# Kernel optimization log

Hardware: AMD Instinct MI355X
Metric: run time of the kernel (lower is better)

Reference implementation:

```python
import jax, jax.numpy as jnp
import numpy as np

N_NODES = 50000
N_EDGES = 800000
N_GRAPHS = 64
D_IN = 96
D_HID = 96
D_OUT = 2
NEG_SLOPE = 0.2


def setup_inputs() -> dict:
    key = jax.random.key(0)
    ks = jax.random.split(key, 9)
    x = jax.random.normal(ks[0], (N_NODES, D_IN), dtype=jnp.float32)
    edge_index = jax.random.randint(ks[1], (2, N_EDGES), 0, N_NODES, dtype=jnp.int32)
    batch = jnp.sort(jax.random.randint(ks[2], (N_NODES,), 0, N_GRAPHS, dtype=jnp.int32))
    s1 = 1.0 / np.sqrt(D_IN)
    s2 = 1.0 / np.sqrt(D_HID)
    W1 = jax.random.normal(ks[3], (D_IN, D_HID), dtype=jnp.float32) * s1
    b1 = jnp.zeros((D_HID,), dtype=jnp.float32)
    W2 = jax.random.normal(ks[4], (D_HID, D_HID), dtype=jnp.float32) * s2
    b2 = jnp.zeros((D_HID,), dtype=jnp.float32)
    Wc = jax.random.normal(ks[5], (D_HID, D_OUT), dtype=jnp.float32) * s2
    bc = jnp.zeros((D_OUT,), dtype=jnp.float32)
    return {"x": x, "edge_index": edge_index, "batch": batch,
            "W1": W1, "b1": b1, "W2": W2, "b2": b2, "Wc": Wc, "bc": bc}


def _gcn_conv(h, W, b, src, dst, n_nodes):
    # GCNConv (Kipf): add self-loops, symmetric deg^-1/2 normalization.
    hW = h @ W  # [N, F]
    deg = jnp.zeros((n_nodes,), dtype=hW.dtype).at[dst].add(1.0) + 1.0  # +1 self-loop
    dinv = jax.lax.rsqrt(deg)
    coef = (dinv[src] * dinv[dst])[:, None]            # [E, 1]
    agg = jnp.zeros_like(hW).at[dst].add(hW[src] * coef)
    out = agg + hW * (dinv * dinv)[:, None] + b        # self-loop term: deg^-1 * hW
    return out


def _leaky(h):
    return jnp.where(h > 0, h, NEG_SLOPE * h)


def reference(x, edge_index, batch, W1, b1, W2, b2, Wc, bc):
    src, dst = edge_index[0], edge_index[1]
    h = _leaky(_gcn_conv(x, W1, b1, src, dst, N_NODES))
    h = _leaky(_gcn_conv(h, W2, b2, src, dst, N_NODES))
    # global_mean_pool over graph ids
    sums = jax.ops.segment_sum(h, batch, num_segments=N_GRAPHS)
    cnts = jax.ops.segment_sum(jnp.ones((N_NODES,), dtype=h.dtype), batch, num_segments=N_GRAPHS)
    pooled = sums / jnp.maximum(cnts, 1.0)[:, None]    # [G, F]
    return pooled @ Wc + bc                             # [G, D_OUT]
```

## Files before the change

### kernel.cpp

```cpp
#include <hip/hip_runtime.h>
#include <hip/hip_fp16.h>

#define NN 50000
#define NE 800000
#define NG 64
#define DF 96
#define SLOPE 0.2f
#define NBK 196
#define EB 196

using half8 = __attribute__((ext_vector_type(8))) _Float16;
using f32x4 = __attribute__((ext_vector_type(4))) float;

__global__ __launch_bounds__(256) void k_hist(const int* __restrict__ dst,
                                              int* __restrict__ hist2d) {
  __shared__ int h[NBK];
  int t = threadIdx.x;
  if (t < NBK) h[t] = 0;
  __syncthreads();
  int base = blockIdx.x * 4096;
  for (int k = 0; k < 16; ++k) {
    int e = base + k * 256 + t;
    if (e < NE) atomicAdd(&h[dst[e] >> 8], 1);
  }
  __syncthreads();
  if (t < NBK) hist2d[blockIdx.x * NBK + t] = h[t];
}

__global__ __launch_bounds__(256) void k_colscan(const int* __restrict__ hist2d,
                                                 int* __restrict__ colpref,
                                                 int* __restrict__ coltotal,
                                                 const int* __restrict__ batch,
                                                 int* __restrict__ gstart) {
  __shared__ int s[256];
  int col = blockIdx.x;
  int b = threadIdx.x;
  int v = (b < EB) ? hist2d[b * NBK + col] : 0;
  s[b] = v;
  __syncthreads();
  for (int o = 1; o < 256; o <<= 1) {
    int u = (b >= o) ? s[b - o] : 0;
    __syncthreads();
    s[b] += u;
    __syncthreads();
  }
  if (b < EB) colpref[b * NBK + col] = s[b] - v;
  if (b == 255) coltotal[col] = s[b];
  if (blockIdx.x == 0 && b <= NG) {
    int g = b, lo = 0, hi = NN;
    while (lo < hi) {
      int mid = (lo + hi) >> 1;
      if (batch[mid] < g) lo = mid + 1; else hi = mid;
    }
    gstart[g] = lo;
  }
}

__global__ __launch_bounds__(256) void k_bin2(const int* __restrict__ src,
                                              const int* __restrict__ dst,
                                              const int* __restrict__ hist2d,
                                              const int* __restrict__ coltotal,
                                              const int* __restrict__ colpref,
                                              int* __restrict__ binned) {
  __shared__ int h[NBK], loff[NBK], cur[NBK], gb[NBK];
  __shared__ int tmp[256];
  __shared__ int stage[4096];
  __shared__ unsigned char sbk[4096];
  int t = threadIdx.x;
  int ctv = (t < NBK) ? coltotal[t] : 0;
  tmp[t] = ctv;
  __syncthreads();
  for (int o = 1; o < 256; o <<= 1) {
    int u = (t >= o) ? tmp[t - o] : 0;
    __syncthreads();
    tmp[t] += u;
    __syncthreads();
  }
  int bbase_t = tmp[t] - ctv;
  if (t < NBK) h[t] = hist2d[blockIdx.x * NBK + t];
  __syncthreads();
  tmp[t] = (t < NBK) ? h[t] : 0;
  __syncthreads();
  for (int o = 1; o < 256; o <<= 1) {
    int u = (t >= o) ? tmp[t - o] : 0;
    __syncthreads();
    tmp[t] += u;
    __syncthreads();
  }
  if (t < NBK) {
    int excl = tmp[t] - h[t];
    loff[t] = excl;
    cur[t] = excl;
    gb[t] = bbase_t + colpref[blockIdx.x * NBK + t];
  }
  __syncthreads();
  int base = blockIdx.x * 4096;
  for (int k = 0; k < 16; ++k) {
    int e = base + k * 256 + t;
    if (e < NE) {
      int d = dst[e];
      int b = d >> 8;
      int p = atomicAdd(&cur[b], 1);
      stage[p] = src[e] | ((d & 255) << 16);
      sbk[p] = (unsigned char)b;
    }
  }
  __syncthreads();
  int tot = min(4096, NE - base);
  for (int i = t; i < tot; i += 256) {
    int b = sbk[i];
    binned[gb[b] + (i - loff[b])] = stage[i];
  }
}

__global__ __launch_bounds__(256) void k_csr(const int* __restrict__ binned,
                                             const int* __restrict__ coltotal,
                                             float* __restrict__ dinv,
                                             int* __restrict__ row_start,
                                             unsigned short* __restrict__ csr_src,
                                             float* __restrict__ partial) {
  __shared__ int h[256], cur[256], tmp[256];
  int t = threadIdx.x;
  int b = blockIdx.x;
  if (b == 0)
    for (int i = t; i < NG * DF; i += 256) partial[i] = 0.f;
  int ctv = (t < NBK) ? coltotal[t] : 0;
  h[t] = ctv;
  tmp[t] = ctv;
  __syncthreads();
  for (int o = 1; o < 256; o <<= 1) {
    int u = (t >= o) ? tmp[t - o] : 0;
    __syncthreads();
    tmp[t] += u;
    __syncthreads();
  }
  int ebeg = tmp[b] - h[b];
  int eend = tmp[b];
  __syncthreads();
  h[t] = 0;
  __syncthreads();
  for (int i = ebeg + t; i < eend; i += 256) atomicAdd(&h[(unsigned)binned[i] >> 16], 1);
  __syncthreads();
  tmp[t] = h[t];
  __syncthreads();
  for (int o = 1; o < 256; o <<= 1) {
    int v = (t >= o) ? tmp[t - o] : 0;
    __syncthreads();
    tmp[t] += v;
    __syncthreads();
  }
  int excl = tmp[t] - h[t];
  int rs = ebeg + excl;
  cur[t] = rs;
  int n = b * 256 + t;
  if (n < NN) {
    row_start[n] = rs;
    dinv[n] = rsqrtf((float)h[t] + 1.0f);
  }
  if (b == NBK - 1 && t == 255) row_start[NN] = NE;
  __syncthreads();
  for (int i = ebeg + t; i < eend; i += 256) {
    int pr = binned[i];
    int p = atomicAdd(&cur[(unsigned)pr >> 16], 1);
    csr_src[p] = (unsigned short)(pr & 0xFFFF);
  }
}

#define WTP 104
template <typename T>
__global__ __launch_bounds__(256) void k_gemm(const T* __restrict__ X,
                                              const float* __restrict__ W,
                                              const float* __restrict__ dinv,
                                              __half* __restrict__ G) {
  __shared__ alignas(16) _Float16 Wt[DF * WTP];
  int t = threadIdx.x;
  for (int i = t; i < DF * DF; i += 256) {
    int k = i / DF, c = i % DF;
    Wt[c * WTP + k] = (_Float16)W[i];
  }
  __syncthreads();

  int wave = t >> 6;
  int lane = t & 63;
  int lrow = lane & 15;
  int kgrp = lane >> 4;
  int rowbase = blockIdx.x * 64 + wave * 16;
  int arow = min(rowbase + lrow, NN - 1);

  half8 a[3];
#pragma unroll
  for (int kt = 0; kt < 3; ++kt) {
    int k0 = kt * 32 + kgrp * 8;
    if constexpr (sizeof(T) == 4) {
      const float4* xp = (const float4*)((const float*)X + (size_t)arow * DF + k0);
      float4 v0 = xp[0], v1 = xp[1];
      a[kt][0] = (_Float16)v0.x; a[kt][1] = (_Float16)v0.y;
      a[kt][2] = (_Float16)v0.z; a[kt][3] = (_Float16)v0.w;
      a[kt][4] = (_Float16)v1.x; a[kt][5] = (_Float16)v1.y;
      a[kt][6] = (_Float16)v1.z; a[kt][7] = (_Float16)v1.w;
    } else {
      a[kt] = *(const half8*)((const _Float16*)X + (size_t)arow * DF + k0);
    }
  }

  float dvv[4];
  int orow0 = rowbase + kgrp * 4;
#pragma unroll
  for (int r = 0; r < 4; ++r)
    dvv[r] = (orow0 + r < NN) ? dinv[orow0 + r] : 0.f;

#pragma unroll
  for (int ct = 0; ct < 6; ++ct) {
    int colbase = ct * 16;
    f32x4 acc = {0.f, 0.f, 0.f, 0.f};
#pragma unroll
    for (int kt = 0; kt < 3; ++kt) {
      half8 b = *(const half8*)&Wt[(colbase + lrow) * WTP + kt * 32 + kgrp * 8];
      acc = __builtin_amdgcn_mfma_f32_16x16x32_f16(a[kt], b, acc, 0, 0, 0);
    }
#pragma unroll
    for (int r = 0; r < 4; ++r) {
      int orow = orow0 + r;
      if (orow < NN)
        G[(size_t)orow * DF + colbase + lrow] = __float2half(acc[r] * dvv[r]);
    }
  }
}

template <int FINAL>
__global__ __launch_bounds__(256) void k_agg(const __half* __restrict__ G,
                                             const float* __restrict__ dinv,
                                             const float* __restrict__ bias,
                                             const int* __restrict__ row_start,
                                             const unsigned short* __restrict__ csr_src,
                                             __half* __restrict__ H,
                                             const int* __restrict__ batch,
                                             float* __restrict__ partial) {
  int lane = threadIdx.x & 15;
  int grp = threadIdx.x >> 4;
  int n = blockIdx.x * 16 + grp;
  const unsigned* rn = (const unsigned*)(G + (size_t)n * DF);
  unsigned su0 = rn[lane], su1 = rn[lane + 16], su2 = rn[lane + 32];
  float2 f0 = __half22float2(*(__half2*)&su0);
  float2 f1 = __half22float2(*(__half2*)&su1);
  float2 f2 = __half22float2(*(__half2*)&su2);
  float a00 = f0.x, a01 = f0.y, a10 = f1.x, a11 = f1.y, a20 = f2.x, a21 = f2.y;

  int s = row_start[n], e = row_start[n + 1];
  for (int j0 = s; j0 < e; j0 += 16) {
    int my = (j0 + lane < e) ? (int)csr_src[j0 + lane] : 0;
    int cnt = min(16, e - j0);
    int jj = 0;
    for (; jj + 8 <= cnt; jj += 8) {
      unsigned u[8][3];
#pragma unroll
      for (int q = 0; q < 8; ++q) {
        int srcn = __shfl(my, jj + q, 16);
        const unsigned* r2 = (const unsigned*)(G + (size_t)srcn * DF);
        u[q][0] = r2[lane];
        u[q][1] = r2[lane + 16];
        u[q][2] = r2[lane + 32];
      }
#pragma unroll
      for (int q = 0; q < 8; ++q) {
        float2 g0 = __half22float2(*(__half2*)&u[q][0]);
        float2 g1 = __half22float2(*(__half2*)&u[q][1]);
        float2 g2 = __half22float2(*(__half2*)&u[q][2]);
        a00 += g0.x; a01 += g0.y;
        a10 += g1.x; a11 += g1.y;
        a20 += g2.x; a21 += g2.y;
      }
    }
    for (; jj < cnt; ++jj) {
      int srcn = __shfl(my, jj, 16);
      const unsigned* r2 = (const unsigned*)(G + (size_t)srcn * DF);
      unsigned v0 = r2[lane], v1 = r2[lane + 16], v2 = r2[lane + 32];
      float2 g0 = __half22float2(*(__half2*)&v0);
      float2 g1 = __half22float2(*(__half2*)&v1);
      float2 g2 = __half22float2(*(__half2*)&v2);
      a00 += g0.x; a01 += g0.y;
      a10 += g1.x; a11 += g1.y;
      a20 += g2.x; a21 += g2.y;
    }
  }
  float dv = dinv[n];
  float2 b0 = *(const float2*)(bias + 2 * lane);
  float2 b1 = *(const float2*)(bias + 2 * lane + 32);
  float2 b2 = *(const float2*)(bias + 2 * lane + 64);
  float v00 = dv * a00 + b0.x, v01 = dv * a01 + b0.y;
  float v10 = dv * a10 + b1.x, v11 = dv * a11 + b1.y;
  float v20 = dv * a20 + b2.x, v21 = dv * a21 + b2.y;
  v00 = v00 > 0.f ? v00 : SLOPE * v00;
  v01 = v01 > 0.f ? v01 : SLOPE * v01;
  v10 = v10 > 0.f ? v10 : SLOPE * v10;
  v11 = v11 > 0.f ? v11 : SLOPE * v11;
  v20 = v20 > 0.f ? v20 : SLOPE * v20;
  v21 = v21 > 0.f ? v21 : SLOPE * v21;

  if (!FINAL) {
    __half2* hp = (__half2*)(H + (size_t)n * DF);
    hp[lane] = __floats2half2_rn(v00, v01);
    hp[lane + 16] = __floats2half2_rn(v10, v11);
    hp[lane + 32] = __floats2half2_rn(v20, v21);
  } else {
    __shared__ float red[16][DF];
    __shared__ int gnode[16];
    red[grp][2 * lane] = v00;
    red[grp][2 * lane + 1] = v01;
    red[grp][32 + 2 * lane] = v10;
    red[grp][33 + 2 * lane] = v11;
    red[grp][64 + 2 * lane] = v20;
    red[grp][65 + 2 * lane] = v21;
    if (lane == 0) gnode[grp] = batch[n];
    __syncthreads();
    int f = threadIdx.x;
    if (f < DF) {
      int g0 = gnode[0], g15 = gnode[15];
      if (g0 == g15) {
        float sum = 0.f;
#pragma unroll
        for (int q = 0; q < 16; ++q) sum += red[q][f];
        atomicAdd(&partial[g0 * DF + f], sum);
      } else {
        for (int g = g0; g <= g15; ++g) {
          float sum = 0.f;
          bool any = false;
          for (int q = 0; q < 16; ++q)
            if (gnode[q] == g) { sum += red[q][f]; any = true; }
          if (any) atomicAdd(&partial[g * DF + f], sum);
        }
      }
    }
  }
}

__global__ __launch_bounds__(128) void k_pool3(const float* __restrict__ partial,
                                               const int* __restrict__ gstart,
                                               const float* __restrict__ Wc,
                                               const float* __restrict__ bc,
                                               float* __restrict__ out) {
  __shared__ float pm[DF];
  int g = blockIdx.x;
  int t = threadIdx.x;
  if (t < DF) {
    float cnt = (float)(gstart[g + 1] - gstart[g]);
    pm[t] = partial[g * DF + t] / fmaxf(cnt, 1.0f);
  }
  __syncthreads();
  if (t < 2) {
    float s = 0.f;
    for (int c = 0; c < DF; ++c) s += pm[c] * Wc[c * 2 + t];
    out[g * 2 + t] = s + bc[t];
  }
}

extern "C" void kernel_launch(void* const* d_in, const int* in_sizes, int n_in,
                              void* d_out, int out_size, void* d_ws, size_t ws_size,
                              hipStream_t stream) {
  const float* x = (const float*)d_in[0];
  const int* ei = (const int*)d_in[1];
  const int* batch = (const int*)d_in[2];
  const float* W1 = (const float*)d_in[3];
  const float* b1 = (const float*)d_in[4];
  const float* W2 = (const float*)d_in[5];
  const float* b2 = (const float*)d_in[6];
  const float* Wc = (const float*)d_in[7];
  const float* bc = (const float*)d_in[8];
  float* out = (float*)d_out;
  const int* srcv = ei;
  const int* dstv = ei + NE;

  char* p = (char*)d_ws;
  auto alloc = [&](size_t bytes) {
    char* r = p;
    p += (bytes + 255) & ~(size_t)255;
    return r;
  };
  int* hist2d = (int*)alloc((size_t)EB * NBK * sizeof(int));
  int* colpref = (int*)alloc((size_t)EB * NBK * sizeof(int));
  int* coltotal = (int*)alloc((size_t)NBK * sizeof(int));
  int* gstart = (int*)alloc((size_t)(NG + 1) * sizeof(int));
  int* row_start = (int*)alloc((size_t)(NN + 1) * sizeof(int));
  int* binned = (int*)alloc((size_t)NE * sizeof(int));
  unsigned short* csr_src = (unsigned short*)alloc((size_t)NE * sizeof(unsigned short));
  float* dinv = (float*)alloc((size_t)NN * sizeof(float));
  __half* g = (__half*)alloc((size_t)NN * DF * sizeof(__half));
  __half* h = (__half*)alloc((size_t)NN * DF * sizeof(__half));
  float* partial = (float*)alloc((size_t)NG * DF * sizeof(float));

  k_hist<<<EB, 256, 0, stream>>>(dstv, hist2d);
  k_colscan<<<NBK, 256, 0, stream>>>(hist2d, colpref, coltotal, batch, gstart);
  k_bin2<<<EB, 256, 0, stream>>>(srcv, dstv, hist2d, coltotal, colpref, binned);
  k_csr<<<NBK, 256, 0, stream>>>(binned, coltotal, dinv, row_start, csr_src, partial);

  const int GB = (NN + 63) / 64;
  k_gemm<float><<<GB, 256, 0, stream>>>(x, W1, dinv, g);
  k_agg<0><<<NN / 16, 256, 0, stream>>>(g, dinv, b1, row_start, csr_src, h, batch, partial);
  k_gemm<__half><<<GB, 256, 0, stream>>>((const __half*)h, W2, dinv, g);
  k_agg<1><<<NN / 16, 256, 0, stream>>>(g, dinv, b2, row_start, csr_src, h, batch, partial);

  k_pool3<<<NG, 128, 0, stream>>>(partial, gstart, Wc, bc, out);
}
```

Measured before the change: 121.9 us.

## Fuse layer-1 aggregation with layer-2 GEMM via shared-memory tile

Merges the first aggregation kernel and the second GEMM into one kernel. Each block aggregates 64 nodes into a shared-memory fp16 tile and then multiplies that tile by W2 with MFMA. This drops one kernel launch and the global write and read of the intermediate H matrix. In exchange, each block now handles four node groups serially, and the larger shared-memory footprint (W2 plus the H tile) may reduce occupancy during the latency-bound gather.

```diff
diff --git a/kernel.cpp b/kernel.cpp
--- a/kernel.cpp
+++ b/kernel.cpp
@@ -167,11 +167,10 @@
 }
 
 #define WTP 104
-template <typename T>
-__global__ __launch_bounds__(256) void k_gemm(const T* __restrict__ X,
-                                              const float* __restrict__ W,
-                                              const float* __restrict__ dinv,
-                                              __half* __restrict__ G) {
+__global__ __launch_bounds__(256) void k_gemm1(const float* __restrict__ X,
+                                               const float* __restrict__ W,
+                                               const float* __restrict__ dinv,
+                                               __half* __restrict__ G) {
   __shared__ alignas(16) _Float16 Wt[DF * WTP];
   int t = threadIdx.x;
   for (int i = t; i < DF * DF; i += 256) {
@@ -191,16 +190,12 @@
 #pragma unroll
   for (int kt = 0; kt < 3; ++kt) {
     int k0 = kt * 32 + kgrp * 8;
-    if constexpr (sizeof(T) == 4) {
-      const float4* xp = (const float4*)((const float*)X + (size_t)arow * DF + k0);
-      float4 v0 = xp[0], v1 = xp[1];
-      a[kt][0] = (_Float16)v0.x; a[kt][1] = (_Float16)v0.y;
-      a[kt][2] = (_Float16)v0.z; a[kt][3] = (_Float16)v0.w;
-      a[kt][4] = (_Float16)v1.x; a[kt][5] = (_Float16)v1.y;
-      a[kt][6] = (_Float16)v1.z; a[kt][7] = (_Float16)v1.w;
-    } else {
-      a[kt] = *(const half8*)((const _Float16*)X + (size_t)arow * DF + k0);
-    }
+    const float4* xp = (const float4*)(X + (size_t)arow * DF + k0);
+    float4 v0 = xp[0], v1 = xp[1];
+    a[kt][0] = (_Float16)v0.x; a[kt][1] = (_Float16)v0.y;
+    a[kt][2] = (_Float16)v0.z; a[kt][3] = (_Float16)v0.w;
+    a[kt][4] = (_Float16)v1.x; a[kt][5] = (_Float16)v1.y;
+    a[kt][6] = (_Float16)v1.z; a[kt][7] = (_Float16)v1.w;
   }
 
   float dvv[4];
@@ -227,15 +222,145 @@
   }
 }
 
-template <int FINAL>
-__global__ __launch_bounds__(256) void k_agg(const __half* __restrict__ G,
-                                             const float* __restrict__ dinv,
-                                             const float* __restrict__ bias,
-                                             const int* __restrict__ row_start,
-                                             const unsigned short* __restrict__ csr_src,
-                                             __half* __restrict__ H,
-                                             const int* __restrict__ batch,
-                                             float* __restrict__ partial) {
+__global__ __launch_bounds__(256) void k_fuse(const __half* __restrict__ G,
+                                              const float* __restrict__ dinv,
+                                              const float* __restrict__ bias,
+                                              const int* __restrict__ row_start,
+                                              const unsigned short* __restrict__ csr_src,
+                                              const float* __restrict__ W2,
+                                              __half* __restrict__ Gout) {
+  __shared__ alignas(16) _Float16 Wt[DF * WTP];
+  __shared__ alignas(16) _Float16 Hs[64 * WTP];
+  int t = threadIdx.x;
+  for (int i = t; i < DF * DF; i += 256) {
+    int k = i / DF, c = i % DF;
+    Wt[c * WTP + k] = (_Float16)W2[i];
+  }
+
+  int lane = t & 15;
+  int grp = t >> 4;
+  int blockbase = blockIdx.x * 64;
+
+  for (int it = 0; it < 4; ++it) {
+    int ln = it * 16 + grp;
+    int n = blockbase + ln;
+    _Float16* hrow = &Hs[ln * WTP];
+    if (n < NN) {
+      const unsigned* rn = (const unsigned*)(G + (size_t)n * DF);
+      unsigned su0 = rn[lane], su1 = rn[lane + 16], su2 = rn[lane + 32];
+      float2 f0 = __half22float2(*(__half2*)&su0);
+      float2 f1 = __half22float2(*(__half2*)&su1);
+      float2 f2 = __half22float2(*(__half2*)&su2);
+      float a00 = f0.x, a01 = f0.y, a10 = f1.x, a11 = f1.y, a20 = f2.x, a21 = f2.y;
+      int s = row_start[n], e = row_start[n + 1];
+      for (int j0 = s; j0 < e; j0 += 16) {
+        int my = (j0 + lane < e) ? (int)csr_src[j0 + lane] : 0;
+        int cnt = min(16, e - j0);
+        int jj = 0;
+        for (; jj + 8 <= cnt; jj += 8) {
+          unsigned u[8][3];
+#pragma unroll
+          for (int q = 0; q < 8; ++q) {
+            int srcn = __shfl(my, jj + q, 16);
+            const unsigned* r2 = (const unsigned*)(G + (size_t)srcn * DF);
+            u[q][0] = r2[lane];
+            u[q][1] = r2[lane + 16];
+            u[q][2] = r2[lane + 32];
+          }
+#pragma unroll
+          for (int q = 0; q < 8; ++q) {
+            float2 g0 = __half22float2(*(__half2*)&u[q][0]);
+            float2 g1 = __half22float2(*(__half2*)&u[q][1]);
+            float2 g2 = __half22float2(*(__half2*)&u[q][2]);
+            a00 += g0.x; a01 += g0.y;
+            a10 += g1.x; a11 += g1.y;
+            a20 += g2.x; a21 += g2.y;
+          }
+        }
+        for (; jj < cnt; ++jj) {
+          int srcn = __shfl(my, jj, 16);
+          const unsigned* r2 = (const unsigned*)(G + (size_t)srcn * DF);
+          unsigned v0 = r2[lane], v1 = r2[lane + 16], v2 = r2[lane + 32];
+          float2 g0 = __half22float2(*(__half2*)&v0);
+          float2 g1 = __half22float2(*(__half2*)&v1);
+          float2 g2 = __half22float2(*(__half2*)&v2);
+          a00 += g0.x; a01 += g0.y;
+          a10 += g1.x; a11 += g1.y;
+          a20 += g2.x; a21 += g2.y;
+        }
+      }
+      float dv = dinv[n];
+      float2 b0 = *(const float2*)(bias + 2 * lane);
+      float2 b1 = *(const float2*)(bias + 2 * lane + 32);
+      float2 b2 = *(const float2*)(bias + 2 * lane + 64);
+      float v00 = dv * a00 + b0.x, v01 = dv * a01 + b0.y;
+      float v10 = dv * a10 + b1.x, v11 = dv * a11 + b1.y;
+      float v20 = dv * a20 + b2.x, v21 = dv * a21 + b2.y;
+      v00 = v00 > 0.f ? v00 : SLOPE * v00;
+      v01 = v01 > 0.f ? v01 : SLOPE * v01;
+      v10 = v10 > 0.f ? v10 : SLOPE * v10;
+      v11 = v11 > 0.f ? v11 : SLOPE * v11;
+      v20 = v20 > 0.f ? v20 : SLOPE * v20;
+      v21 = v21 > 0.f ? v21 : SLOPE * v21;
+      hrow[2 * lane] = (_Float16)v00;
+      hrow[2 * lane + 1] = (_Float16)v01;
+      hrow[32 + 2 * lane] = (_Float16)v10;
+      hrow[33 + 2 * lane] = (_Float16)v11;
+      hrow[64 + 2 * lane] = (_Float16)v20;
+      hrow[65 + 2 * lane] = (_Float16)v21;
+    } else {
+      hrow[2 * lane] = (_Float16)0.f;
+      hrow[2 * lane + 1] = (_Float16)0.f;
+      hrow[32 + 2 * lane] = (_Float16)0.f;
+      hrow[33 + 2 * lane] = (_Float16)0.f;
+      hrow[64 + 2 * lane] = (_Float16)0.f;
+      hrow[65 + 2 * lane] = (_Float16)0.f;
+    }
+  }
+  __syncthreads();
+
+  int wave = t >> 6;
+  int l64 = t & 63;
+  int lrow = l64 & 15;
+  int kgrp = l64 >> 4;
+  int lr0 = wave * 16 + lrow;
+
+  half8 a[3];
+#pragma unroll
+  for (int kt = 0; kt < 3; ++kt)
+    a[kt] = *(const half8*)&Hs[lr0 * WTP + kt * 32 + kgrp * 8];
+
+  float dvv[4];
+  int orow0 = blockbase + wave * 16 + kgrp * 4;
+#pragma unroll
+  for (int r = 0; r < 4; ++r)
+    dvv[r] = (orow0 + r < NN) ? dinv[orow0 + r] : 0.f;
+
+#pragma unroll
+  for (int ct = 0; ct < 6; ++ct) {
+    int colbase = ct * 16;
+    f32x4 acc = {0.f, 0.f, 0.f, 0.f};
+#pragma unroll
+    for (int kt = 0; kt < 3; ++kt) {
+      half8 b = *(const half8*)&Wt[(colbase + lrow) * WTP + kt * 32 + kgrp * 8];
+      acc = __builtin_amdgcn_mfma_f32_16x16x32_f16(a[kt], b, acc, 0, 0, 0);
+    }
+#pragma unroll
+    for (int r = 0; r < 4; ++r) {
+      int orow = orow0 + r;
+      if (orow < NN)
+        Gout[(size_t)orow * DF + colbase + lrow] = __float2half(acc[r] * dvv[r]);
+    }
+  }
+}
+
+__global__ __launch_bounds__(256) void k_agg1(const __half* __restrict__ G,
+                                              const float* __restrict__ dinv,
+                                              const float* __restrict__ bias,
+                                              const int* __restrict__ row_start,
+                                              const unsigned short* __restrict__ csr_src,
+                                              const int* __restrict__ batch,
+                                              float* __restrict__ partial) {
   int lane = threadIdx.x & 15;
   int grp = threadIdx.x >> 4;
   int n = blockIdx.x * 16 + grp;
@@ -297,38 +422,31 @@
   v20 = v20 > 0.f ? v20 : SLOPE * v20;
   v21 = v21 > 0.f ? v21 : SLOPE * v21;
 
-  if (!FINAL) {
-    __half2* hp = (__half2*)(H + (size_t)n * DF);
-    hp[lane] = __floats2half2_rn(v00, v01);
-    hp[lane + 16] = __floats2half2_rn(v10, v11);
-    hp[lane + 32] = __floats2half2_rn(v20, v21);
-  } else {
-    __shared__ float red[16][DF];
-    __shared__ int gnode[16];
-    red[grp][2 * lane] = v00;
-    red[grp][2 * lane + 1] = v01;
-    red[grp][32 + 2 * lane] = v10;
-    red[grp][33 + 2 * lane] = v11;
-    red[grp][64 + 2 * lane] = v20;
-    red[grp][65 + 2 * lane] = v21;
-    if (lane == 0) gnode[grp] = batch[n];
-    __syncthreads();
-    int f = threadIdx.x;
-    if (f < DF) {
-      int g0 = gnode[0], g15 = gnode[15];
-      if (g0 == g15) {
+  __shared__ float red[16][DF];
+  __shared__ int gnode[16];
+  red[grp][2 * lane] = v00;
+  red[grp][2 * lane + 1] = v01;
+  red[grp][32 + 2 * lane] = v10;
+  red[grp][33 + 2 * lane] = v11;
+  red[grp][64 + 2 * lane] = v20;
+  red[grp][65 + 2 * lane] = v21;
+  if (lane == 0) gnode[grp] = batch[n];
+  __syncthreads();
+  int f = threadIdx.x;
+  if (f < DF) {
+    int g0 = gnode[0], g15 = gnode[15];
+    if (g0 == g15) {
+      float sum = 0.f;
+#pragma unroll
+      for (int q = 0; q < 16; ++q) sum += red[q][f];
+      atomicAdd(&partial[g0 * DF + f], sum);
+    } else {
+      for (int g = g0; g <= g15; ++g) {
         float sum = 0.f;
-#pragma unroll
-        for (int q = 0; q < 16; ++q) sum += red[q][f];
-        atomicAdd(&partial[g0 * DF + f], sum);
-      } else {
-        for (int g = g0; g <= g15; ++g) {
-          float sum = 0.f;
-          bool any = false;
-          for (int q = 0; q < 16; ++q)
-            if (gnode[q] == g) { sum += red[q][f]; any = true; }
-          if (any) atomicAdd(&partial[g * DF + f], sum);
-        }
+        bool any = false;
+        for (int q = 0; q < 16; ++q)
+          if (gnode[q] == g) { sum += red[q][f]; any = true; }
+        if (any) atomicAdd(&partial[g * DF + f], sum);
       }
     }
   }
@@ -385,7 +503,7 @@
   unsigned short* csr_src = (unsigned short*)alloc((size_t)NE * sizeof(unsigned short));
   float* dinv = (float*)alloc((size_t)NN * sizeof(float));
   __half* g = (__half*)alloc((size_t)NN * DF * sizeof(__half));
-  __half* h = (__half*)alloc((size_t)NN * DF * sizeof(__half));
+  __half* g2 = (__half*)alloc((size_t)NN * DF * sizeof(__half));
   float* partial = (float*)alloc((size_t)NG * DF * sizeof(float));
 
   k_hist<<<EB, 256, 0, stream>>>(dstv, hist2d);
@@ -394,10 +512,9 @@
   k_csr<<<NBK, 256, 0, stream>>>(binned, coltotal, dinv, row_start, csr_src, partial);
 
   const int GB = (NN + 63) / 64;
-  k_gemm<float><<<GB, 256, 0, stream>>>(x, W1, dinv, g);
-  k_agg<0><<<NN / 16, 256, 0, stream>>>(g, dinv, b1, row_start, csr_src, h, batch, partial);
-  k_gemm<__half><<<GB, 256, 0, stream>>>((const __half*)h, W2, dinv, g);
-  k_agg<1><<<NN / 16, 256, 0, stream>>>(g, dinv, b2, row_start, csr_src, h, batch, partial);
+  k_gemm1<<<GB, 256, 0, stream>>>(x, W1, dinv, g);
+  k_fuse<<<GB, 256, 0, stream>>>(g, dinv, b1, row_start, csr_src, W2, g2);
+  k_agg1<<<NN / 16, 256, 0, stream>>>(g2, dinv, b2, row_start, csr_src, batch, partial);
 
   k_pool3<<<NG, 128, 0, stream>>>(partial, gstart, Wc, bc, out);
 }
```

Result: no change. 122.7 us (+0.7%).
